# Performance work log

Hardware: AMD Instinct MI355X
Metric: run time of the kernel (lower is better)

Reference implementation:

```python
import jax, jax.numpy as jnp
import numpy as np

B, S, H, DH, E = 8, 2048, 1024, 4096, 8
ALPHA = 0.5
LN_EPS = 1e-5


def setup_inputs() -> dict:
    key = jax.random.key(0)
    ks = jax.random.split(key, 8)
    sc = 0.02
    return {
        "x": jax.random.normal(ks[0], (B, S, H), jnp.float32),
        "We1": jax.random.normal(ks[1], (E, H, DH), jnp.float32) * sc,
        "be1": jnp.zeros((E, DH), jnp.float32),
        "We2": jax.random.normal(ks[2], (E, DH, H), jnp.float32) * sc,
        "be2": jnp.zeros((E, H), jnp.float32),
        "Wq": jax.random.normal(ks[3], (H, H), jnp.float32) * sc,
        "bq": jnp.zeros((H,), jnp.float32),
        "Wk": jax.random.normal(ks[4], (H, H), jnp.float32) * sc,
        "bk": jnp.zeros((H,), jnp.float32),
        "Wv": jax.random.normal(ks[5], (H, H), jnp.float32) * sc,
        "bv": jnp.zeros((H,), jnp.float32),
        "ln_g": jnp.ones((H,), jnp.float32),
        "ln_b": jnp.zeros((H,), jnp.float32),
        "current_expert_idx": E - 1,
    }


def _boosting_forward(x, We1, be1, We2, be2, Wq, bq, Wk, bk, Wv, bv, ln_g, ln_b, cur):
    sg = jax.lax.stop_gradient
    n = cur + 1  # static Python int: number of experts executed
    boost = sg(x)  # boost_input = x.detach()
    outs = []
    for i in range(n):
        h = jax.nn.relu(jnp.einsum("bsh,hf->bsf", boost, We1[i]) + be1[i])
        eo = jnp.einsum("bsf,fh->bsh", h, We2[i]) + be2[i]  # dropout = identity (eval)
        if i < n - 1:
            eo = sg(eo)  # earlier experts detached
        boost = boost + ALPHA * eo
        outs.append(eo)
    stacked = jnp.stack(outs, axis=2)  # [B,S,n,H]
    q = jnp.einsum("bsh,hd->bsd", x, Wq) + bq          # [B,S,H]
    k = jnp.einsum("bseh,hd->bsed", stacked, Wk) + bk  # [B,S,n,H]
    v = jnp.einsum("bseh,hd->bsed", stacked, Wv) + bv
    scores = jnp.einsum("bsd,bsed->bse", q, k) / jnp.sqrt(jnp.asarray(H, x.dtype))
    w = jax.nn.softmax(scores, axis=-1)                # [B,S,n]
    fused = jnp.einsum("bse,bsed->bsd", w, v)          # [B,S,H]
    y = x + fused
    mu = jnp.mean(y, axis=-1, keepdims=True)
    var = jnp.mean(jnp.square(y - mu), axis=-1, keepdims=True)
    return (y - mu) * jax.lax.rsqrt(var + LN_EPS) * ln_g + ln_b


def reference(x, We1, be1, We2, be2, Wq, bq, Wk, bk, Wv, bv, ln_g, ln_b, current_expert_idx):
    return _boosting_forward(x, We1, be1, We2, be2, Wq, bq, Wk, bk, Wv, bv, ln_g, ln_b, int(current_expert_idx))
```

## Files before the change

### kernel.cpp

```cpp
#include <hip/hip_runtime.h>
#include <math.h>

typedef __bf16 bf16_t;
typedef __bf16 bf16x8 __attribute__((ext_vector_type(8)));
typedef __bf16 bf16x4 __attribute__((ext_vector_type(4)));
typedef float f32x4 __attribute__((ext_vector_type(4)));
typedef unsigned int u32;

static constexpr int kBd = 8, kS = 2048, kH = 1024, kDH = 4096, kE = 8;
static constexpr int kM = kBd * kS;
static constexpr float kScale = 0.03125f;

__device__ __forceinline__ void gload_lds16(const void* g, void* l) {
  __builtin_amdgcn_global_load_lds(
      (const __attribute__((address_space(1))) u32*)g,
      (__attribute__((address_space(3))) u32*)l, 16, 0, 0);
}

__global__ __launch_bounds__(256) void cvt_flat_kernel(const float* __restrict__ in,
                                                       bf16_t* __restrict__ out, int n4) {
  int i = blockIdx.x * 256 + threadIdx.x;
  if (i >= n4) return;
  f32x4 v = *(const f32x4*)(in + (size_t)i * 4);
  bf16x4 o;
#pragma unroll
  for (int j = 0; j < 4; ++j) o[j] = (bf16_t)v[j];
  *(bf16x4*)(out + (size_t)i * 4) = o;
}

__global__ __launch_bounds__(256) void transpose_cvt_kernel(
    const float* __restrict__ in, bf16_t* __restrict__ out, int R, int C) {
  __shared__ float tile[32][33];
  int tx = threadIdx.x & 31, ty = threadIdx.x >> 5;
  int c0 = blockIdx.x * 32, r0 = blockIdx.y * 32;
#pragma unroll
  for (int yy = 0; yy < 4; ++yy)
    tile[ty + yy * 8][tx] = in[(size_t)(r0 + ty + yy * 8) * C + c0 + tx];
  __syncthreads();
#pragma unroll
  for (int yy = 0; yy < 4; ++yy)
    out[(size_t)(c0 + ty + yy * 8) * R + r0 + tx] = (bf16_t)tile[tx][ty + yy * 8];
}

template <int MODE>
__global__ __launch_bounds__(512, 2) void gemm256_kernel(
    const bf16_t* __restrict__ A, const bf16_t* __restrict__ Bt,
    int M, int N, int K, int nwg,
    const float* __restrict__ bias,
    bf16_t* __restrict__ outb,
    const bf16_t* __restrict__ bin_b, bf16_t* __restrict__ bout_b,
    bf16_t* __restrict__ stacked,
    const float* __restrict__ xres,
    const int* __restrict__ curp, int expert_i) {
  if ((MODE == 0 || MODE == 4) && expert_i > *curp) return;
  extern __shared__ char lds_buf[];
  char* Abase = lds_buf;
  char* Bbase = lds_buf + 98304;
  const int tid = threadIdx.x;
  const int lane = tid & 63, wid = tid >> 6;
  const int wr = wid >> 2, wc = wid & 3;
  const int fr = lane & 15, fh = lane >> 4;
  const int lane_swz = (fr * 64 + fh * 16) ^ ((fr >> 3) << 5);
  const int bid = blockIdx.x;
  const int wg = (bid & 7) * (nwg >> 3) + (bid >> 3);
  const int nNb = N >> 8;
  const int chsz = 8 * nNb;
  const int chunk = wg / chsz, loc = wg % chsz;
  const int m0 = (chunk * 8 + (loc & 7)) << 8;
  const int n0 = (loc >> 3) << 8;
  int grow[2], gcol[2];
#pragma unroll
  for (int j = 0; j < 2; ++j) {
    int L = (j * 512 + tid) * 16;
    int Lp = L ^ (((L >> 9) & 1) << 5);
    int s = Lp >> 10;
    grow[j] = ((s >> 1) << 4) + ((Lp >> 6) & 15);
    gcol[j] = ((s & 1) << 5) + (((Lp >> 4) & 3) << 3);
  }
  const bf16_t* sA[2] = {A + (size_t)(m0 + grow[0]) * K + gcol[0],
                         A + (size_t)(m0 + grow[1]) * K + gcol[1]};
  const bf16_t* sB[2] = {Bt + (size_t)(n0 + grow[0]) * K + gcol[0],
                         Bt + (size_t)(n0 + grow[1]) * K + gcol[1]};
  const size_t rstep = (size_t)128 * K;

#define STAGE(SP, BASE, tau, h)                                               \
  {                                                                           \
    char* d_ = (BASE) + ((h) << 14) + (wid << 10);                            \
    gload_lds16(SP[0] + (size_t)(h)*rstep + (size_t)(tau)*64, d_);            \
    gload_lds16(SP[1] + (size_t)(h)*rstep + (size_t)(tau)*64, d_ + 8192);     \
  }
#define STAGE_A(buf, t, h) STAGE(sA, Abase + (buf)*32768, (t), (h))
#define STAGE_B(t, h) STAGE(sB, Bbase + (((t)&1) << 15), (t), (h))
#define SB0() __builtin_amdgcn_sched_barrier(0)

  const int bq = (wc & 1) * 4;

  f32x4 acc[8][4] = {};
  const int NT = K >> 6;

#define QUAD(p, af)                                                            \
  __builtin_amdgcn_s_setprio(1);                                               \
  _Pragma("unroll") for (int nf = 0; nf < 4; ++nf) {                           \
    acc[2 * (p)][nf] = __builtin_amdgcn_mfma_f32_16x16x32_bf16(                \
        af[0], b[nf][0], acc[2 * (p)][nf], 0, 0, 0);                           \
    acc[2 * (p)][nf] = __builtin_amdgcn_mfma_f32_16x16x32_bf16(                \
        af[1], b[nf][1], acc[2 * (p)][nf], 0, 0, 0);                           \
    acc[2 * (p) + 1][nf] = __builtin_amdgcn_mfma_f32_16x16x32_bf16(            \
        af[2], b[nf][0], acc[2 * (p) + 1][nf], 0, 0, 0);                       \
    acc[2 * (p) + 1][nf] = __builtin_amdgcn_mfma_f32_16x16x32_bf16(            \
        af[3], b[nf][1], acc[2 * (p) + 1][nf], 0, 0, 0);                       \
  }                                                                            \
  __builtin_amdgcn_s_setprio(0);

  STAGE_A(0, 0, 0); STAGE_A(0, 0, 1);
  STAGE_B(0, 0); STAGE_B(0, 1);
  STAGE_A(1, 1, 0); STAGE_A(1, 1, 1);
  STAGE_B(1, 0); STAGE_B(1, 1);
  asm volatile("s_waitcnt vmcnt(8)" ::: "memory");
  __builtin_amdgcn_s_barrier();

  int am0 = 0;
  for (int t = 0; t < NT; ++t) {
    int am2 = am0 + 2; if (am2 >= 3) am2 -= 3;
    const char* Ar = Abase + am0 * 32768 + (wr << 14) + lane_swz;
    const char* Br = Bbase + ((t & 1) << 15) + ((wc >> 1) << 14) + lane_swz;
    bf16x8 b[4][2], a01[8], a23[8];
    const bool st = (t + 2 < NT);
#pragma unroll
    for (int nf = 0; nf < 4; ++nf)
#pragma unroll
      for (int kk = 0; kk < 2; ++kk)
        b[nf][kk] = *(const bf16x8*)(Br + ((bq + nf) * 2 + kk) * 1024);
    SB0();
#pragma unroll
    for (int i = 0; i < 8; ++i) a01[i] = *(const bf16x8*)(Ar + i * 1024);
    SB0();
    if (st) { STAGE_A(am2, t + 2, 0); STAGE_A(am2, t + 2, 1); }
    SB0();
    QUAD(0, (&a01[0]));
#pragma unroll
    for (int i = 0; i < 8; ++i) a23[i] = *(const bf16x8*)(Ar + (8 + i) * 1024);
    SB0();
    QUAD(1, (&a01[4]));
    asm volatile("s_waitcnt lgkmcnt(8)" ::: "memory");
    SB0();
    if (st) { STAGE_B(t + 2, 0); STAGE_B(t + 2, 1); }
    SB0();
    QUAD(2, (&a23[0]));
    QUAD(3, (&a23[4]));
    if (t < NT - 2) {
      asm volatile("s_waitcnt vmcnt(8)" ::: "memory");
    } else {
      asm volatile("s_waitcnt vmcnt(0)" ::: "memory");
    }
    __builtin_amdgcn_s_barrier();
    am0 = am0 + 1; if (am0 >= 3) am0 -= 3;
  }
#undef QUAD
#undef STAGE
#undef STAGE_A
#undef STAGE_B
#undef SB0

#pragma unroll
  for (int nf = 0; nf < 4; ++nf) {
    const int col = n0 + wc * 64 + nf * 16 + fr;
    const float bv = bias ? bias[col] : 0.0f;
#pragma unroll
    for (int mf = 0; mf < 8; ++mf) {
#pragma unroll
      for (int r = 0; r < 4; ++r) {
        const int row = m0 + wr * 128 + mf * 16 + fh * 4 + r;
        const size_t idx = (size_t)row * N + col;
        float v = acc[mf][nf][r] + bv;
        if (MODE == 0) {
          outb[idx] = (bf16_t)(v > 0.0f ? v : 0.0f);
        } else if (MODE == 2) {
          outb[idx] = (bf16_t)v;
        } else if (MODE == 4) {
          float nb2 = (float)bin_b[idx] + 0.5f * v;
          bout_b[idx] = (bf16_t)nb2;
          stacked[idx] = (bf16_t)v;
        } else {
          outb[idx] = (bf16_t)(v + xres[idx]);
        }
      }
    }
  }
}

__global__ __launch_bounds__(256) void scores_mix_kernel(
    const bf16_t* __restrict__ qk, const bf16_t* __restrict__ q,
    const float* __restrict__ bk, const bf16_t* __restrict__ stacked,
    bf16_t* __restrict__ mix, const int* __restrict__ curp) {
  const int n = *curp + 1;
  int lane = threadIdx.x & 63, wave = threadIdx.x >> 6;
  int m = blockIdx.x * 4 + wave;
  size_t base = (size_t)m * kH + lane * 16;
  int c0 = lane * 16;
  bf16x8 qk0 = *(const bf16x8*)(qk + base);
  bf16x8 qk1 = *(const bf16x8*)(qk + base + 8);
  bf16x8 q0 = *(const bf16x8*)(q + base);
  bf16x8 q1 = *(const bf16x8*)(q + base + 8);
  float sc[kE + 1];
  bf16x8 eo0[kE], eo1[kE];
#pragma unroll
  for (int e = 0; e < kE; ++e) {
    sc[e] = 0.0f;
    if (e < n) {
      size_t sb = (size_t)e * kM * kH + base;
      eo0[e] = *(const bf16x8*)(stacked + sb);
      eo1[e] = *(const bf16x8*)(stacked + sb + 8);
      float d = 0.0f;
#pragma unroll
      for (int j = 0; j < 8; ++j)
        d += (float)eo0[e][j] * (float)qk0[j] + (float)eo1[e][j] * (float)qk1[j];
      sc[e] = d;
    }
  }
  {
    float qb = 0.0f;
#pragma unroll
    for (int j = 0; j < 8; ++j)
      qb += (float)q0[j] * bk[c0 + j] + (float)q1[j] * bk[c0 + 8 + j];
    sc[kE] = qb;
  }
#pragma unroll
  for (int off = 32; off >= 1; off >>= 1)
#pragma unroll
    for (int e = 0; e <= kE; ++e) sc[e] += __shfl_xor(sc[e], off, 64);
  float s[kE];
  float mx = -1e30f;
#pragma unroll
  for (int e = 0; e < kE; ++e)
    if (e < n) {
      s[e] = (sc[e] + sc[kE]) * kScale;
      mx = fmaxf(mx, s[e]);
    }
  float Z = 0.0f;
#pragma unroll
  for (int e = 0; e < kE; ++e)
    if (e < n) {
      s[e] = expf(s[e] - mx);
      Z += s[e];
    }
  float inv = 1.0f / Z;
  float mv[16];
#pragma unroll
  for (int j = 0; j < 16; ++j) mv[j] = 0.0f;
#pragma unroll
  for (int e = 0; e < kE; ++e)
    if (e < n) {
      float w = s[e] * inv;
#pragma unroll
      for (int j = 0; j < 8; ++j) {
        mv[j] += w * (float)eo0[e][j];
        mv[8 + j] += w * (float)eo1[e][j];
      }
    }
  bf16x8 o0, o1;
#pragma unroll
  for (int j = 0; j < 8; ++j) {
    o0[j] = (bf16_t)mv[j];
    o1[j] = (bf16_t)mv[8 + j];
  }
  *(bf16x8*)(mix + base) = o0;
  *(bf16x8*)(mix + base + 8) = o1;
}

__global__ __launch_bounds__(256) void layernorm_kernel(
    const bf16_t* __restrict__ y, const float* __restrict__ g,
    const float* __restrict__ b, float* __restrict__ out) {
  int lane = threadIdx.x & 63, wave = threadIdx.x >> 6;
  int m = blockIdx.x * 4 + wave;
  size_t base = (size_t)m * kH + lane * 16;
  bf16x8 v0 = *(const bf16x8*)(y + base);
  bf16x8 v1 = *(const bf16x8*)(y + base + 8);
  float vf[16];
#pragma unroll
  for (int j = 0; j < 8; ++j) {
    vf[j] = (float)v0[j];
    vf[8 + j] = (float)v1[j];
  }
  float s = 0.0f, s2 = 0.0f;
#pragma unroll
  for (int j = 0; j < 16; ++j) {
    s += vf[j];
    s2 += vf[j] * vf[j];
  }
#pragma unroll
  for (int off = 32; off >= 1; off >>= 1) {
    s += __shfl_xor(s, off, 64);
    s2 += __shfl_xor(s2, off, 64);
  }
  float mu = s * (1.0f / kH);
  float var = s2 * (1.0f / kH) - mu * mu;
  float rs = rsqrtf(var + 1e-5f);
  int c0 = lane * 16;
#pragma unroll
  for (int j = 0; j < 4; ++j) {
    f32x4 gg = *(const f32x4*)(g + c0 + j * 4);
    f32x4 bb = *(const f32x4*)(b + c0 + j * 4);
    f32x4 o;
#pragma unroll
    for (int t = 0; t < 4; ++t) o[t] = (vf[j * 4 + t] - mu) * rs * gg[t] + bb[t];
    *(f32x4*)(out + base + j * 4) = o;
  }
}

extern "C" void kernel_launch(void* const* d_in, const int* in_sizes, int n_in,
                              void* d_out, int out_size, void* d_ws, size_t ws_size,
                              hipStream_t stream) {
  const float* x = (const float*)d_in[0];
  const float* We1 = (const float*)d_in[1];
  const float* be1 = (const float*)d_in[2];
  const float* We2 = (const float*)d_in[3];
  const float* be2 = (const float*)d_in[4];
  const float* Wq = (const float*)d_in[5];
  const float* bq = (const float*)d_in[6];
  const float* Wk = (const float*)d_in[7];
  const float* bk = (const float*)d_in[8];
  const float* Wv = (const float*)d_in[9];
  const float* bv = (const float*)d_in[10];
  const float* ln_g = (const float*)d_in[11];
  const float* ln_b = (const float*)d_in[12];
  const int* curp = (const int*)d_in[13];
  float* out = (float*)d_out;

  char* ws = (char*)d_ws;
  const size_t MB = 1ull << 20;
  bf16_t* stacked = (bf16_t*)(ws);
  bf16_t* xb = (bf16_t*)(ws + 256 * MB);
  bf16_t* boostb = (bf16_t*)(ws + 288 * MB);
  bf16_t* wA = (bf16_t*)(ws + 320 * MB);
  bf16_t* wB = (bf16_t*)(ws + 328 * MB);
  bf16_t* WqT = (bf16_t*)(ws + 336 * MB);
  bf16_t* WkC = (bf16_t*)(ws + 338 * MB);
  bf16_t* WvT = (bf16_t*)(ws + 340 * MB);
  char* dyn = ws + 342 * MB;
  size_t rem = ws_size > 342 * MB ? ws_size - 342 * MB : 0;
  int nchunk;
  if (rem >= 128 * MB) nchunk = 1;
  else if (rem >= 64 * MB) nchunk = 2;
  else nchunk = 4;
  bf16_t* hbuf = (bf16_t*)dyn;
  bf16_t* qb_ = hbuf;
  bf16_t* qkb = boostb;
  bf16_t* mixb = xb;
  bf16_t* ybf = (bf16_t*)ws;

  const int Mc = kM / nchunk;
  const size_t MH = (size_t)kM * kH;
  const u32 kLds = 163840;
  dim3 blk(256), blk5(512);

  cvt_flat_kernel<<<(kM * kH) / 1024, blk, 0, stream>>>(x, xb, (kM * kH) / 4);
  cvt_flat_kernel<<<(kH * kH) / 1024, blk, 0, stream>>>(Wk, WkC, (kH * kH) / 4);
  transpose_cvt_kernel<<<dim3(kH / 32, kH / 32), blk, 0, stream>>>(Wq, WqT, kH, kH);
  transpose_cvt_kernel<<<dim3(kH / 32, kH / 32), blk, 0, stream>>>(Wv, WvT, kH, kH);

  for (int i = 0; i < kE; ++i) {
    transpose_cvt_kernel<<<dim3(kDH / 32, kH / 32), blk, 0, stream>>>(
        We1 + (size_t)i * kH * kDH, wA, kH, kDH);
    transpose_cvt_kernel<<<dim3(kH / 32, kDH / 32), blk, 0, stream>>>(
        We2 + (size_t)i * kH * kDH, wB, kDH, kH);
    for (int c = 0; c < nchunk; ++c) {
      const size_t ro = (size_t)c * Mc * kH;
      const bf16_t* Ain = ((i == 0) ? xb : boostb) + ro;
      {
        int nwg = (Mc / 256) * (kDH / 256);
        gemm256_kernel<0><<<nwg, blk5, kLds, stream>>>(
            Ain, wA, Mc, kDH, kH, nwg, be1 + (size_t)i * kDH, hbuf,
            nullptr, nullptr, nullptr, nullptr, curp, i);
      }
      int nwg = (Mc / 256) * (kH / 256);
      const bf16_t* binb = ((i == 0) ? xb : boostb) + ro;
      gemm256_kernel<4><<<nwg, blk5, kLds, stream>>>(
          hbuf, wB, Mc, kH, kDH, nwg, be2 + (size_t)i * kH, nullptr,
          binb, boostb + ro, stacked + (size_t)i * MH + ro, nullptr, curp, i);
    }
  }

  const int nwgH = (kM / 256) * (kH / 256);
  gemm256_kernel<2><<<nwgH, blk5, kLds, stream>>>(
      xb, WqT, kM, kH, kH, nwgH, bq, qb_,
      nullptr, nullptr, nullptr, nullptr, curp, 0);
  gemm256_kernel<2><<<nwgH, blk5, kLds, stream>>>(
      qb_, WkC, kM, kH, kH, nwgH, nullptr, qkb,
      nullptr, nullptr, nullptr, nullptr, curp, 0);
  scores_mix_kernel<<<dim3(kM / 4), blk, 0, stream>>>(qkb, qb_, bk, stacked, mixb, curp);
  gemm256_kernel<3><<<nwgH, blk5, kLds, stream>>>(
      mixb, WvT, kM, kH, kH, nwgH, bv, ybf,
      nullptr, nullptr, nullptr, x, curp, 0);
  layernorm_kernel<<<dim3(kM / 4), blk, 0, stream>>>(ybf, ln_g, ln_b, out);
}
```

Before: 2.905 ms.

## Replace 256x256 GEMM tile kernel with smaller 128x128 tile, 4-wave kernel

Swaps the 512-thread 256x256x64 bf16 MFMA GEMM for a 256-thread 128x128x32 variant with a triple-buffered LDS ring, a simpler XOR swizzle and 48KB LDS, so more workgroups fit per CU. Every GEMM launch in the expert loop and the attention projections uses the new kernel. This gives up per-tile data reuse and the hand-interleaved load/MFMA schedule in exchange for more occupancy and simpler pipelining, and it raises global/L2 traffic per FLOP.

```diff
diff --git a/kernel.cpp b/kernel.cpp
--- a/kernel.cpp
+++ b/kernel.cpp
@@ -43,7 +43,7 @@
 }
 
 template <int MODE>
-__global__ __launch_bounds__(512, 2) void gemm256_kernel(
+__global__ __launch_bounds__(256, 4) void gemm128_kernel(
     const bf16_t* __restrict__ A, const bf16_t* __restrict__ Bt,
     int M, int N, int K, int nwg,
     const float* __restrict__ bias,
@@ -55,111 +55,74 @@
   if ((MODE == 0 || MODE == 4) && expert_i > *curp) return;
   extern __shared__ char lds_buf[];
   char* Abase = lds_buf;
-  char* Bbase = lds_buf + 98304;
+  char* Bbase = lds_buf + 24576;
   const int tid = threadIdx.x;
   const int lane = tid & 63, wid = tid >> 6;
-  const int wr = wid >> 2, wc = wid & 3;
+  const int wr = wid >> 1, wc = wid & 1;
   const int fr = lane & 15, fh = lane >> 4;
-  const int lane_swz = (fr * 64 + fh * 16) ^ ((fr >> 3) << 5);
+  const int lane_off = fr * 64 + ((fh ^ (fr & 3)) << 4);
   const int bid = blockIdx.x;
   const int wg = (bid & 7) * (nwg >> 3) + (bid >> 3);
-  const int nNb = N >> 8;
+  const int nNb = N >> 7;
   const int chsz = 8 * nNb;
   const int chunk = wg / chsz, loc = wg % chsz;
-  const int m0 = (chunk * 8 + (loc & 7)) << 8;
-  const int n0 = (loc >> 3) << 8;
-  int grow[2], gcol[2];
-#pragma unroll
-  for (int j = 0; j < 2; ++j) {
-    int L = (j * 512 + tid) * 16;
-    int Lp = L ^ (((L >> 9) & 1) << 5);
-    int s = Lp >> 10;
-    grow[j] = ((s >> 1) << 4) + ((Lp >> 6) & 15);
-    gcol[j] = ((s & 1) << 5) + (((Lp >> 4) & 3) << 3);
-  }
-  const bf16_t* sA[2] = {A + (size_t)(m0 + grow[0]) * K + gcol[0],
-                         A + (size_t)(m0 + grow[1]) * K + gcol[1]};
-  const bf16_t* sB[2] = {Bt + (size_t)(n0 + grow[0]) * K + gcol[0],
-                         Bt + (size_t)(n0 + grow[1]) * K + gcol[1]};
-  const size_t rstep = (size_t)128 * K;
-
-#define STAGE(SP, BASE, tau, h)                                               \
+  const int m0 = (chunk * 8 + (loc & 7)) << 7;
+  const int n0 = (loc >> 3) << 7;
+  const int grow_ = tid >> 2;
+  const int gcol_ = (((tid & 3) ^ ((tid >> 2) & 3)) << 3);
+  const bf16_t* sA[2] = {A + (size_t)(m0 + grow_) * K + gcol_,
+                         A + (size_t)(m0 + grow_ + 64) * K + gcol_};
+  const bf16_t* sB[2] = {Bt + (size_t)(n0 + grow_) * K + gcol_,
+                         Bt + (size_t)(n0 + grow_ + 64) * K + gcol_};
+
+#define STAGE(SP, BASE, buf, t)                                               \
   {                                                                           \
-    char* d_ = (BASE) + ((h) << 14) + (wid << 10);                            \
-    gload_lds16(SP[0] + (size_t)(h)*rstep + (size_t)(tau)*64, d_);            \
-    gload_lds16(SP[1] + (size_t)(h)*rstep + (size_t)(tau)*64, d_ + 8192);     \
-  }
-#define STAGE_A(buf, t, h) STAGE(sA, Abase + (buf)*32768, (t), (h))
-#define STAGE_B(t, h) STAGE(sB, Bbase + (((t)&1) << 15), (t), (h))
+    char* d_ = (BASE) + (buf)*8192 + (wid << 10);                             \
+    gload_lds16(SP[0] + (size_t)(t)*32, d_);                                  \
+    gload_lds16(SP[1] + (size_t)(t)*32, d_ + 4096);                           \
+  }
 #define SB0() __builtin_amdgcn_sched_barrier(0)
 
-  const int bq = (wc & 1) * 4;
-
-  f32x4 acc[8][4] = {};
-  const int NT = K >> 6;
-
-#define QUAD(p, af)                                                            \
-  __builtin_amdgcn_s_setprio(1);                                               \
-  _Pragma("unroll") for (int nf = 0; nf < 4; ++nf) {                           \
-    acc[2 * (p)][nf] = __builtin_amdgcn_mfma_f32_16x16x32_bf16(                \
-        af[0], b[nf][0], acc[2 * (p)][nf], 0, 0, 0);                           \
-    acc[2 * (p)][nf] = __builtin_amdgcn_mfma_f32_16x16x32_bf16(                \
-        af[1], b[nf][1], acc[2 * (p)][nf], 0, 0, 0);                           \
-    acc[2 * (p) + 1][nf] = __builtin_amdgcn_mfma_f32_16x16x32_bf16(            \
-        af[2], b[nf][0], acc[2 * (p) + 1][nf], 0, 0, 0);                       \
-    acc[2 * (p) + 1][nf] = __builtin_amdgcn_mfma_f32_16x16x32_bf16(            \
-        af[3], b[nf][1], acc[2 * (p) + 1][nf], 0, 0, 0);                       \
-  }                                                                            \
-  __builtin_amdgcn_s_setprio(0);
-
-  STAGE_A(0, 0, 0); STAGE_A(0, 0, 1);
-  STAGE_B(0, 0); STAGE_B(0, 1);
-  STAGE_A(1, 1, 0); STAGE_A(1, 1, 1);
-  STAGE_B(1, 0); STAGE_B(1, 1);
-  asm volatile("s_waitcnt vmcnt(8)" ::: "memory");
+  f32x4 acc[4][4] = {};
+  const int NT = K >> 5;
+
+  STAGE(sA, Abase, 0, 0); STAGE(sB, Bbase, 0, 0);
+  STAGE(sA, Abase, 1, 1); STAGE(sB, Bbase, 1, 1);
+  asm volatile("s_waitcnt vmcnt(4)" ::: "memory");
   __builtin_amdgcn_s_barrier();
 
-  int am0 = 0;
+  int am0 = 0, am2 = 2;
   for (int t = 0; t < NT; ++t) {
-    int am2 = am0 + 2; if (am2 >= 3) am2 -= 3;
-    const char* Ar = Abase + am0 * 32768 + (wr << 14) + lane_swz;
-    const char* Br = Bbase + ((t & 1) << 15) + ((wc >> 1) << 14) + lane_swz;
-    bf16x8 b[4][2], a01[8], a23[8];
-    const bool st = (t + 2 < NT);
-#pragma unroll
-    for (int nf = 0; nf < 4; ++nf)
-#pragma unroll
-      for (int kk = 0; kk < 2; ++kk)
-        b[nf][kk] = *(const bf16x8*)(Br + ((bq + nf) * 2 + kk) * 1024);
+    const char* Ar = Abase + am0 * 8192 + (wr << 12) + lane_off;
+    const char* Br = Bbase + am0 * 8192 + (wc << 12) + lane_off;
+    bf16x8 a[4], b[4];
+#pragma unroll
+    for (int nf = 0; nf < 4; ++nf) b[nf] = *(const bf16x8*)(Br + nf * 1024);
+#pragma unroll
+    for (int mf = 0; mf < 4; ++mf) a[mf] = *(const bf16x8*)(Ar + mf * 1024);
     SB0();
-#pragma unroll
-    for (int i = 0; i < 8; ++i) a01[i] = *(const bf16x8*)(Ar + i * 1024);
+    if (t + 2 < NT) {
+      STAGE(sA, Abase, am2, t + 2);
+      STAGE(sB, Bbase, am2, t + 2);
+    }
     SB0();
-    if (st) { STAGE_A(am2, t + 2, 0); STAGE_A(am2, t + 2, 1); }
-    SB0();
-    QUAD(0, (&a01[0]));
-#pragma unroll
-    for (int i = 0; i < 8; ++i) a23[i] = *(const bf16x8*)(Ar + (8 + i) * 1024);
-    SB0();
-    QUAD(1, (&a01[4]));
-    asm volatile("s_waitcnt lgkmcnt(8)" ::: "memory");
-    SB0();
-    if (st) { STAGE_B(t + 2, 0); STAGE_B(t + 2, 1); }
-    SB0();
-    QUAD(2, (&a23[0]));
-    QUAD(3, (&a23[4]));
+    __builtin_amdgcn_s_setprio(1);
+#pragma unroll
+    for (int mf = 0; mf < 4; ++mf)
+#pragma unroll
+      for (int nf = 0; nf < 4; ++nf)
+        acc[mf][nf] = __builtin_amdgcn_mfma_f32_16x16x32_bf16(a[mf], b[nf], acc[mf][nf], 0, 0, 0);
+    __builtin_amdgcn_s_setprio(0);
     if (t < NT - 2) {
-      asm volatile("s_waitcnt vmcnt(8)" ::: "memory");
+      asm volatile("s_waitcnt vmcnt(4)" ::: "memory");
     } else {
       asm volatile("s_waitcnt vmcnt(0)" ::: "memory");
     }
     __builtin_amdgcn_s_barrier();
-    am0 = am0 + 1; if (am0 >= 3) am0 -= 3;
-  }
-#undef QUAD
+    am0 = (am0 + 1 >= 3) ? 0 : am0 + 1;
+    am2 = (am2 + 1 >= 3) ? 0 : am2 + 1;
+  }
 #undef STAGE
-#undef STAGE_A
-#undef STAGE_B
 #undef SB0
 
 #pragma unroll
@@ -167,10 +130,10 @@
     const int col = n0 + wc * 64 + nf * 16 + fr;
     const float bv = bias ? bias[col] : 0.0f;
 #pragma unroll
-    for (int mf = 0; mf < 8; ++mf) {
+    for (int mf = 0; mf < 4; ++mf) {
 #pragma unroll
       for (int r = 0; r < 4; ++r) {
-        const int row = m0 + wr * 128 + mf * 16 + fh * 4 + r;
+        const int row = m0 + wr * 64 + mf * 16 + fh * 4 + r;
         const size_t idx = (size_t)row * N + col;
         float v = acc[mf][nf][r] + bv;
         if (MODE == 0) {
@@ -351,8 +314,8 @@
 
   const int Mc = kM / nchunk;
   const size_t MH = (size_t)kM * kH;
-  const u32 kLds = 163840;
-  dim3 blk(256), blk5(512);
+  const u32 kLds = 49152;
+  dim3 blk(256);
 
   cvt_flat_kernel<<<(kM * kH) / 1024, blk, 0, stream>>>(x, xb, (kM * kH) / 4);
   cvt_flat_kernel<<<(kH * kH) / 1024, blk, 0, stream>>>(Wk, WkC, (kH * kH) / 4);
@@ -368,28 +331,28 @@
       const size_t ro = (size_t)c * Mc * kH;
       const bf16_t* Ain = ((i == 0) ? xb : boostb) + ro;
       {
-        int nwg = (Mc / 256) * (kDH / 256);
-        gemm256_kernel<0><<<nwg, blk5, kLds, stream>>>(
+        int nwg = (Mc / 128) * (kDH / 128);
+        gemm128_kernel<0><<<nwg, blk, kLds, stream>>>(
             Ain, wA, Mc, kDH, kH, nwg, be1 + (size_t)i * kDH, hbuf,
             nullptr, nullptr, nullptr, nullptr, curp, i);
       }
-      int nwg = (Mc / 256) * (kH / 256);
+      int nwg = (Mc / 128) * (kH / 128);
       const bf16_t* binb = ((i == 0) ? xb : boostb) + ro;
-      gemm256_kernel<4><<<nwg, blk5, kLds, stream>>>(
+      gemm128_kernel<4><<<nwg, blk, kLds, stream>>>(
           hbuf, wB, Mc, kH, kDH, nwg, be2 + (size_t)i * kH, nullptr,
           binb, boostb + ro, stacked + (size_t)i * MH + ro, nullptr, curp, i);
     }
   }
 
-  const int nwgH = (kM / 256) * (kH / 256);
-  gemm256_kernel<2><<<nwgH, blk5, kLds, stream>>>(
+  const int nwgH = (kM / 128) * (kH / 128);
+  gemm128_kernel<2><<<nwgH, blk, kLds, stream>>>(
       xb, WqT, kM, kH, kH, nwgH, bq, qb_,
       nullptr, nullptr, nullptr, nullptr, curp, 0);
-  gemm256_kernel<2><<<nwgH, blk5, kLds, stream>>>(
+  gemm128_kernel<2><<<nwgH, blk, kLds, stream>>>(
       qb_, WkC, kM, kH, kH, nwgH, nullptr, qkb,
       nullptr, nullptr, nullptr, nullptr, curp, 0);
   scores_mix_kernel<<<dim3(kM / 4), blk, 0, stream>>>(qkb, qb_, bk, stacked, mixb, curp);
-  gemm256_kernel<3><<<nwgH, blk5, kLds, stream>>>(
+  gemm128_kernel<3><<<nwgH, blk, kLds, stream>>>(
       mixb, WvT, kM, kH, kH, nwgH, bv, ybf,
       nullptr, nullptr, nullptr, x, curp, 0);
   layernorm_kernel<<<dim3(kM / 4), blk, 0, stream>>>(ybf, ln_g, ln_b, out);
```

Measured after the change: 3.286 ms. 13.1% more time.
